# Performance work log

Hardware: AMD Instinct MI355X
Metric: run time of the kernel (lower is better)

Reference implementation:

```python
import jax, jax.numpy as jnp
import numpy as np

N = 1 << 19          # active voxels
CIN, COUT = 64, 128
STRIDE = 2
B, T, H, W = 4, 8, 512, 512   # batch_size and spatial_shape [T,H,W]
EPS = 1e-5


def setup_inputs() -> dict:
    key = jax.random.key(0)
    k1, k2, k3, k4, k5, k6 = jax.random.split(key, 6)
    features = jax.random.normal(k1, (N, CIN), dtype=jnp.float32)
    b = jax.random.randint(k2, (N,), 0, B)
    t = jax.random.randint(k3, (N,), 0, T)
    y = jax.random.randint(k4, (N,), 0, H)
    x = jax.random.randint(k5, (N,), 0, W)
    indices = jnp.stack([b, t, y, x], axis=1).astype(jnp.int32)  # [N,4]
    weight = jax.random.normal(k6, (CIN, COUT), dtype=jnp.float32) / np.sqrt(CIN)
    gamma = jnp.ones((COUT,), dtype=jnp.float32)
    beta = jnp.zeros((COUT,), dtype=jnp.float32)
    return {"features": features, "indices": indices, "weight": weight,
            "gamma": gamma, "beta": beta}


def reference(features, indices, weight, gamma, beta):
    # --- sort_sparse_tensor: lexicographic sort via linear index (b,t,y,x) ---
    idx = indices.astype(jnp.int32)
    lin = (idx[:, 0] * (T * H * W) + idx[:, 1] * (H * W)
           + idx[:, 2] * W + idx[:, 3])
    order = jnp.argsort(lin)
    feats = features[order]          # [N, CIN] gathered in sorted order
    sidx = idx[order]                # [N, 4]
    # --- kernel-1 strided sparse conv: only voxels with y%s==0 and x%s==0
    #     survive; per-voxel 1x1 GEMM (bias=False) ---
    mask = (sidx[:, 2] % STRIDE == 0) & (sidx[:, 3] % STRIDE == 0)  # [N]
    out = feats @ weight             # [N, COUT]
    # --- SparseGroupNorm == LayerNorm over channels ---
    mu = jnp.mean(out, axis=-1, keepdims=True)
    var = jnp.mean(jnp.square(out - mu), axis=-1, keepdims=True)
    ln = (out - mu) * jax.lax.rsqrt(var + EPS) * gamma + beta
    # fixed-shape stand-in for spconv's compaction: zero invalid rows,
    # mark their indices -1 (valid rows carry identical math to spconv).
    out_f = jnp.where(mask[:, None], ln, 0.0)
    new_idx = sidx.at[:, 2].set(sidx[:, 2] // STRIDE)
    new_idx = new_idx.at[:, 3].set(new_idx[:, 3] // STRIDE)
    new_idx = jnp.where(mask[:, None], new_idx, -1)
    return out_f, new_idx
```

## Files before the change

### kernel.cpp

```cpp
#include <hip/hip_runtime.h>
#include <stdint.h>

#define N_VOX   (1 << 19)
#define CIN     64
#define COUT    128
#define BIN_SHIFT 5
#define BINS    (1 << 18)
#define OFF_BITS 6
#define BPB     128
#define NBLK    (BINS / BPB)
#define NTILES  256
#define PCAP    384
#define EPSV    1e-5f

typedef float f32x4 __attribute__((ext_vector_type(4)));

static __device__ __forceinline__ void nt_store4(float* p, f32x4 v) {
    __builtin_nontemporal_store(v, (f32x4*)p);
}


#define CLR_INTS (BINS + 4 + 2 * NTILES)
#define CLR_4    (CLR_INTS / 4 + 1)

__global__ void k_clear(int* __restrict__ p) {
    int t = blockIdx.x * 256 + threadIdx.x;
    if (t * 4 < CLR_INTS) *(int4*)&p[t * 4] = make_int4(0, 0, 0, 0);
}

__global__ void k_hist(const int* __restrict__ idx, unsigned* __restrict__ packed,
                       int* __restrict__ hist) {
    int j = blockIdx.x * 256 + threadIdx.x;
    int4 v = *(const int4*)&idx[j * 4];
    int lin = ((v.x * 8 + v.y) * 512 + v.z) * 512 + v.w;
    int off = atomicAdd(&hist[lin >> BIN_SHIFT], 1);
    packed[j] = ((unsigned)lin << OFF_BITS) | (unsigned)off;
}

__global__ __launch_bounds__(256) void k_scan(
    const int* __restrict__ hist, int* __restrict__ cursor,
    unsigned long long* __restrict__ tiles, int* __restrict__ ticket) {
    __shared__ int stile;
    __shared__ int wsums[4];
    __shared__ int sprefix;
    int tid = threadIdx.x;
    if (tid == 0) stile = atomicAdd(ticket, 1);
    __syncthreads();
    int tile = stile;
    int base = tile * 1024 + tid * 4;
    int4 v = *(const int4*)&hist[base];
    int t3 = v.x + v.y + v.z + v.w;
    int lane = tid & 63, w = tid >> 6;
    int incl = t3;
    #pragma unroll
    for (int off = 1; off < 64; off <<= 1) {
        int u = __shfl_up(incl, off);
        if (lane >= off) incl += u;
    }
    if (lane == 63) wsums[w] = incl;
    __syncthreads();
    int woff = (w > 0 ? wsums[0] : 0) + (w > 1 ? wsums[1] : 0) + (w > 2 ? wsums[2] : 0);
    int total = wsums[0] + wsums[1] + wsums[2] + wsums[3];
    int texcl = woff + incl - t3;
    if (tid == 0) {
        unsigned long long st = (tile == 0) ? 2ull : 1ull;
        atomicExch(&tiles[tile], (st << 40) | (unsigned long long)(unsigned)total);
        int pfx = 0;
        if (tile > 0) {
            int p = tile - 1;
            while (true) {
                unsigned long long d = atomicAdd(&tiles[p], 0ull);
                unsigned long long st2 = d >> 40;
                if (st2 == 0) { __builtin_amdgcn_s_sleep(2); continue; }
                pfx += (int)(unsigned)(d & 0xFFFFFFFFull);
                if (st2 == 2ull) break;
                p--;
            }
            atomicExch(&tiles[tile],
                       (2ull << 40) | (unsigned long long)(unsigned)(pfx + total));
        }
        sprefix = pfx;
    }
    __syncthreads();
    int prefix = sprefix + texcl;
    int4 e;
    e.x = prefix;
    e.y = prefix + v.x;
    e.z = prefix + v.x + v.y;
    e.w = prefix + v.x + v.y + v.z;
    *(int4*)&cursor[base] = e;
}

__global__ void k_scatter(const unsigned* __restrict__ packed, const int* __restrict__ cursor,
                          uint2* __restrict__ recs) {
    int j = blockIdx.x * 256 + threadIdx.x;
    unsigned p = packed[j];
    unsigned lin = p >> OFF_BITS;
    int pos = cursor[lin >> BIN_SHIFT] + (int)(p & ((1u << OFF_BITS) - 1u));
    recs[pos] = make_uint2(lin, (unsigned)j);
}

__global__ __launch_bounds__(256) void k_mega(
    const float* __restrict__ feats, const float* __restrict__ weight,
    const float* __restrict__ gamma, const float* __restrict__ beta,
    const int* __restrict__ hist, const int* __restrict__ cursor,
    const uint2* __restrict__ recs, float* __restrict__ out) {
    __shared__ float featb[4][8][CIN];
    __shared__ unsigned slin[PCAP];
    __shared__ int sperm[PCAP];
    __shared__ unsigned short vpos[PCAP];
    __shared__ int wsum[4];

    int tid = threadIdx.x;
    int w = tid >> 6, lane = tid & 63;
    int B0 = blockIdx.x * BPB;
    int p0 = cursor[B0];
    int p1 = (B0 + BPB < BINS) ? cursor[B0 + BPB] : N_VOX;
    int npos = p1 - p0;

    for (int lp = tid; lp < npos; lp += 256) {
        uint2 r = recs[p0 + lp];
        slin[lp] = r.x;
        sperm[lp] = (int)r.y;
    }
    __syncthreads();

    int c = 0, ls = 0;
    if (tid < BPB) {
        c = hist[B0 + tid];
        ls = cursor[B0 + tid] - p0;
    }
    if (c >= 2) {
        for (int i = 1; i < c; i++) {
            unsigned lj = slin[ls + i];
            int pj = sperm[ls + i];
            unsigned long long kj = ((unsigned long long)lj << 19) | (unsigned)pj;
            int m = i - 1;
            while (m >= 0) {
                unsigned lm = slin[ls + m];
                int pm = sperm[ls + m];
                unsigned long long km = ((unsigned long long)lm << 19) | (unsigned)pm;
                if (km <= kj) break;
                slin[ls + m + 1] = lm;
                sperm[ls + m + 1] = pm;
                m--;
            }
            slin[ls + m + 1] = lj;
            sperm[ls + m + 1] = pj;
        }
    }
    int myv = 0;
    for (int i = 0; i < c; i++)
        myv += ((slin[ls + i] & 0x201u) == 0u) ? 1 : 0;
    int incl = myv;
    #pragma unroll
    for (int off = 1; off < 64; off <<= 1) {
        int u = __shfl_up(incl, off);
        if (lane >= off) incl += u;
    }
    if (lane == 63) wsum[w] = incl;
    __syncthreads();
    int s0 = wsum[0], s1 = wsum[1], s2 = wsum[2], s3 = wsum[3];
    int nv = s0 + s1 + s2 + s3;
    int woff = (w > 0 ? s0 : 0) + (w > 1 ? s1 : 0) + (w > 2 ? s2 : 0);

    int half = lane >> 5, l32 = lane & 31;
    float* oidx = out + (size_t)N_VOX * COUT;

    {
        f32x4 z = {0.f, 0.f, 0.f, 0.f};
        for (int lp = w * 2 + half; lp < npos; lp += 8) {
            if (slin[lp] & 0x201u)
                nt_store4(&out[(size_t)(p0 + lp) * COUT + l32 * 4], z);
        }
        f32x4 mi = {-1.f, -1.f, -1.f, -1.f};
        for (int lp = tid; lp < npos; lp += 256) {
            if (slin[lp] & 0x201u)
                nt_store4(&oidx[(size_t)(p0 + lp) * 4], mi);
        }
    }

    int basev = woff + incl - myv;
    for (int i = 0; i < c; i++) {
        int lp = ls + i;
        if ((slin[lp] & 0x201u) == 0u) vpos[basev++] = (unsigned short)lp;
    }
    __syncthreads();

    if (nv == 0) return;
    const f32x4* Wg4 = (const f32x4*)weight;
    f32x4 gv = *(const f32x4*)&gamma[l32 * 4];
    f32x4 bv = *(const f32x4*)&beta[l32 * 4];

    for (int m0 = 0; m0 < nv; m0 += 32) {
        int mb = m0 + w * 8;
        if (mb >= nv) continue;
        #pragma unroll
        for (int i = 0; i < 8; i++) {
            int m = mb + i;
            int lp = vpos[(m < nv) ? m : 0];
            featb[w][i][lane] = feats[(size_t)sperm[lp] * CIN + lane];
        }

        f32x4 acc[4];
        #pragma unroll
        for (int i = 0; i < 4; i++) acc[i] = (f32x4){0.f, 0.f, 0.f, 0.f};

        #pragma unroll 4
        for (int k0 = 0; k0 < CIN; k0 += 4) {
            f32x4 wv0 = Wg4[(k0 + 0) * 32 + l32];
            f32x4 wv1 = Wg4[(k0 + 1) * 32 + l32];
            f32x4 wv2 = Wg4[(k0 + 2) * 32 + l32];
            f32x4 wv3 = Wg4[(k0 + 3) * 32 + l32];
            #pragma unroll
            for (int ii = 0; ii < 4; ii++) {
                float4 f = *(float4*)&featb[w][2 * ii + half][k0];
                acc[ii] += f.x * wv0;
                acc[ii] += f.y * wv1;
                acc[ii] += f.z * wv2;
                acc[ii] += f.w * wv3;
            }
        }

        #pragma unroll
        for (int ii = 0; ii < 4; ii++) {
            int m = mb + 2 * ii + half;
            f32x4 a = acc[ii];
            float sm = a.x + a.y + a.z + a.w;
            float sq = a.x * a.x + a.y * a.y + a.z * a.z + a.w * a.w;
            #pragma unroll
            for (int off = 16; off > 0; off >>= 1) {
                sm += __shfl_xor(sm, off);
                sq += __shfl_xor(sq, off);
            }
            float mean = sm * (1.0f / COUT);
            float var  = fmaxf(sq * (1.0f / COUT) - mean * mean, 0.0f);
            float rstd = rsqrtf(var + EPSV);
            if (m < nv) {
                int lp = vpos[m];
                int pos = p0 + lp;
                f32x4 o = (a - mean) * rstd * gv + bv;
                nt_store4(&out[(size_t)pos * COUT + l32 * 4], o);
                if (l32 == 0) {
                    unsigned lin = slin[lp];
                    f32x4 ni;
                    ni.x = (float)(lin >> 21);
                    ni.y = (float)((lin >> 18) & 7u);
                    ni.z = (float)(((lin >> 9) & 511u) >> 1);
                    ni.w = (float)((lin & 511u) >> 1);
                    nt_store4(&oidx[(size_t)pos * 4], ni);
                }
            }
        }
    }
}

extern "C" void kernel_launch(void* const* d_in, const int* in_sizes, int n_in,
                              void* d_out, int out_size, void* d_ws, size_t ws_size,
                              hipStream_t stream) {
    const float* feats  = (const float*)d_in[0];
    const int*   idx    = (const int*)d_in[1];
    const float* weight = (const float*)d_in[2];
    const float* gamma  = (const float*)d_in[3];
    const float* beta   = (const float*)d_in[4];
    float* out = (float*)d_out;

    int* ws = (int*)d_ws;
    int*                hist   = ws;
    int*                ticket = ws + BINS;
    unsigned long long* tiles  = (unsigned long long*)(ws + BINS + 4);
    int*                cursor = ws + BINS + 4 + 2 * NTILES;
    unsigned*           packed = (unsigned*)(cursor + BINS);
    uint2*              recs   = (uint2*)(packed + N_VOX);

    k_clear<<<(CLR_4 + 255) / 256, 256, 0, stream>>>(ws);
    k_hist<<<N_VOX / 256, 256, 0, stream>>>(idx, packed, hist);
    k_scan<<<NTILES, 256, 0, stream>>>(hist, cursor, tiles, ticket);
    k_scatter<<<N_VOX / 256, 256, 0, stream>>>(packed, cursor, recs);
    k_mega<<<NBLK, 256, 0, stream>>>(feats, weight, gamma, beta,
                                     hist, cursor, recs, out);
}
```

Measured before the change: 145.1 us.

## Partition sorted positions per wave with ballot compaction and interleave zero-row stores

Each wave now owns a contiguous quarter of the block's sorted positions and builds its own valid-voxel list with ballot and popcount, replacing the block-wide shuffle scan and its barrier. Index output for valid and invalid rows is written in one coalesced pass. Zero rows for invalid voxels are written between GEMM tiles in position order rather than in a separate pass beforehand. This cuts a barrier and improves write locality, but load balance across waves now depends on how valid voxels are spread within each quarter, and the per-wave list size of 96 is an assumed cap.

```diff
diff --git a/kernel.cpp b/kernel.cpp
--- a/kernel.cpp
+++ b/kernel.cpp
@@ -108,8 +108,7 @@
     __shared__ float featb[4][8][CIN];
     __shared__ unsigned slin[PCAP];
     __shared__ int sperm[PCAP];
-    __shared__ unsigned short vpos[PCAP];
-    __shared__ int wsum[4];
+    __shared__ unsigned short wvpos[4][96];
 
     int tid = threadIdx.x;
     int w = tid >> 6, lane = tid & 63;
@@ -149,62 +148,61 @@
             sperm[ls + m + 1] = pj;
         }
     }
-    int myv = 0;
-    for (int i = 0; i < c; i++)
-        myv += ((slin[ls + i] & 0x201u) == 0u) ? 1 : 0;
-    int incl = myv;
-    #pragma unroll
-    for (int off = 1; off < 64; off <<= 1) {
-        int u = __shfl_up(incl, off);
-        if (lane >= off) incl += u;
-    }
-    if (lane == 63) wsum[w] = incl;
-    __syncthreads();
-    int s0 = wsum[0], s1 = wsum[1], s2 = wsum[2], s3 = wsum[3];
-    int nv = s0 + s1 + s2 + s3;
-    int woff = (w > 0 ? s0 : 0) + (w > 1 ? s1 : 0) + (w > 2 ? s2 : 0);
-
+    __syncthreads();
+
+    int Q = (npos + 3) >> 2;
+    int r0 = w * Q;
+    int r1 = min(npos, r0 + Q);
     int half = lane >> 5, l32 = lane & 31;
     float* oidx = out + (size_t)N_VOX * COUT;
 
-    {
-        f32x4 z = {0.f, 0.f, 0.f, 0.f};
-        for (int lp = w * 2 + half; lp < npos; lp += 8) {
-            if (slin[lp] & 0x201u)
-                nt_store4(&out[(size_t)(p0 + lp) * COUT + l32 * 4], z);
-        }
-        f32x4 mi = {-1.f, -1.f, -1.f, -1.f};
-        for (int lp = tid; lp < npos; lp += 256) {
-            if (slin[lp] & 0x201u)
-                nt_store4(&oidx[(size_t)(p0 + lp) * 4], mi);
-        }
-    }
-
-    int basev = woff + incl - myv;
-    for (int i = 0; i < c; i++) {
-        int lp = ls + i;
-        if ((slin[lp] & 0x201u) == 0u) vpos[basev++] = (unsigned short)lp;
-    }
-    __syncthreads();
-
-    if (nv == 0) return;
+    int wnv = 0;
+    for (int base = r0; base < r1; base += 64) {
+        int lp = base + lane;
+        bool valid = (lp < r1) && ((slin[lp] & 0x201u) == 0u);
+        unsigned long long bv = __ballot(valid);
+        int rank = __builtin_popcountll(bv & ((1ull << lane) - 1ull));
+        if (valid) wvpos[w][wnv + rank] = (unsigned short)lp;
+        wnv += __builtin_popcountll(bv);
+    }
+
+    for (int lp = r0 + lane; lp < r1; lp += 64) {
+        unsigned lin = slin[lp];
+        f32x4 ni;
+        if ((lin & 0x201u) == 0u) {
+            ni.x = (float)(lin >> 21);
+            ni.y = (float)((lin >> 18) & 7u);
+            ni.z = (float)(((lin >> 9) & 511u) >> 1);
+            ni.w = (float)((lin & 511u) >> 1);
+        } else {
+            ni = (f32x4){-1.f, -1.f, -1.f, -1.f};
+        }
+        nt_store4(&oidx[(size_t)(p0 + lp) * 4], ni);
+    }
+
+    f32x4 z = {0.f, 0.f, 0.f, 0.f};
+    if (wnv == 0) {
+        for (int lp = r0 + half; lp < r1; lp += 2)
+            nt_store4(&out[(size_t)(p0 + lp) * COUT + l32 * 4], z);
+        return;
+    }
+
     const f32x4* Wg4 = (const f32x4*)weight;
     f32x4 gv = *(const f32x4*)&gamma[l32 * 4];
-    f32x4 bv = *(const f32x4*)&beta[l32 * 4];
-
-    for (int m0 = 0; m0 < nv; m0 += 32) {
-        int mb = m0 + w * 8;
-        if (mb >= nv) continue;
+    f32x4 bvv = *(const f32x4*)&beta[l32 * 4];
+    int wcur = r0;
+
+    for (int mb = 0; mb < wnv; mb += 8) {
         #pragma unroll
         for (int i = 0; i < 8; i++) {
             int m = mb + i;
-            int lp = vpos[(m < nv) ? m : 0];
+            int lp = wvpos[w][(m < wnv) ? m : 0];
             featb[w][i][lane] = feats[(size_t)sperm[lp] * CIN + lane];
         }
 
         f32x4 acc[4];
         #pragma unroll
-        for (int i = 0; i < 4; i++) acc[i] = (f32x4){0.f, 0.f, 0.f, 0.f};
+        for (int i = 0; i < 4; i++) acc[i] = z;
 
         #pragma unroll 4
         for (int k0 = 0; k0 < CIN; k0 += 4) {
@@ -236,22 +234,19 @@
             float mean = sm * (1.0f / COUT);
             float var  = fmaxf(sq * (1.0f / COUT) - mean * mean, 0.0f);
             float rstd = rsqrtf(var + EPSV);
-            if (m < nv) {
-                int lp = vpos[m];
-                int pos = p0 + lp;
-                f32x4 o = (a - mean) * rstd * gv + bv;
+            if (m < wnv) {
+                int pos = p0 + wvpos[w][m];
+                f32x4 o = (a - mean) * rstd * gv + bvv;
                 nt_store4(&out[(size_t)pos * COUT + l32 * 4], o);
-                if (l32 == 0) {
-                    unsigned lin = slin[lp];
-                    f32x4 ni;
-                    ni.x = (float)(lin >> 21);
-                    ni.y = (float)((lin >> 18) & 7u);
-                    ni.z = (float)(((lin >> 9) & 511u) >> 1);
-                    ni.w = (float)((lin & 511u) >> 1);
-                    nt_store4(&oidx[(size_t)pos * 4], ni);
-                }
-            }
-        }
+            }
+        }
+
+        int wnext = (mb + 8 < wnv) ? (int)wvpos[w][mb + 8] : r1;
+        for (int lp = wcur + half; lp < wnext; lp += 2) {
+            if (slin[lp] & 0x201u)
+                nt_store4(&out[(size_t)(p0 + lp) * COUT + l32 * 4], z);
+        }
+        wcur = wnext;
     }
 }
 
```

Result: faster. 142.1 us (-2.1%).
